# Kernel tuning notes

Hardware: AMD Instinct MI355X
Metric: run time of the kernel (lower is better)

Reference implementation:

```python
import jax, jax.numpy as jnp
import numpy as np

DIM = 512
NUM_HEADS = 8
HEAD_DIM = DIM // NUM_HEADS
SCALE = HEAD_DIM ** -0.5


def setup_inputs() -> dict:
    key = jax.random.key(0)
    k1, k2, k3, k4 = jax.random.split(key, 4)
    x = jax.random.normal(k1, (2, 4096, DIM), dtype=jnp.float32)
    # Linear weights stored as (in, out) for x @ W; torch Linear(dim, 3*dim, bias=False)
    w_qkv = jax.random.normal(k2, (DIM, 3 * DIM), dtype=jnp.float32) * (DIM ** -0.5)
    w_proj = jax.random.normal(k3, (DIM, DIM), dtype=jnp.float32) * (DIM ** -0.5)
    b_proj = jax.random.normal(k4, (DIM,), dtype=jnp.float32) * 0.02
    return {"x": x, "w_qkv": w_qkv, "w_proj": w_proj, "b_proj": b_proj}


def reference(x, w_qkv, w_proj, b_proj):
    B, N, C = x.shape
    qkv = (x @ w_qkv).reshape(B, N, 3, NUM_HEADS, HEAD_DIM)
    qkv = jnp.transpose(qkv, (2, 0, 3, 1, 4))  # (3, B, H, N, hd)
    q, k, v = qkv[0], qkv[1], qkv[2]
    attn = jnp.einsum("bhnd,bhmd->bhnm", q, k) * SCALE
    attn = jax.nn.softmax(attn, axis=-1)
    out = jnp.einsum("bhnm,bhmd->bhnd", attn, v)
    out = jnp.transpose(out, (0, 2, 1, 3)).reshape(B, N, C)
    return out @ w_proj + b_proj
```

## Files before the change

### kernel.cpp

```cpp
#include <hip/hip_runtime.h>
#include <hip/hip_bf16.h>
#include <stdint.h>
#include <math.h>

#define NC3 1536
#define QSCALE 0.18033688011111907f
#define KSPLIT 2

typedef __attribute__((ext_vector_type(8))) short short8;
typedef __attribute__((ext_vector_type(4))) short short4v;
typedef __attribute__((ext_vector_type(4))) float f32x4;
typedef __attribute__((ext_vector_type(16))) float f32x16;
typedef __attribute__((ext_vector_type(8))) _Float16 f16x8;
typedef __attribute__((ext_vector_type(2))) __fp16 fp16x2;

static __device__ __forceinline__ short f2bf(float f) {
    union { __hip_bfloat16 h; short s; } u;
    u.h = __float2bfloat16(f);
    return u.s;
}
static __device__ __forceinline__ float bf2f(short s) {
    return __uint_as_float(((unsigned)(unsigned short)s) << 16);
}
static __device__ __forceinline__ unsigned bfpack(float a, float b) {
    unsigned ua = (__float_as_uint(a) + 0x8000u) >> 16;
    unsigned ub = (__float_as_uint(b) + 0x8000u) & 0xffff0000u;
    return ua | ub;
}
static __device__ __forceinline__ unsigned hpack(float a, float b) {
    union { fp16x2 h; unsigned u; } c;
    c.h = __builtin_amdgcn_cvt_pkrtz(a, b);
    return c.u;
}

#define GLD_LDS(g, l)                                                          \
    __builtin_amdgcn_global_load_lds(                                          \
        (const __attribute__((address_space(1))) void*)(g),                    \
        (__attribute__((address_space(3))) void*)(l), 16, 0, 0)

__global__ __launch_bounds__(256) void cast_f32_bf16(const float* __restrict__ src,
                                                     short* __restrict__ dst, int n4) {
    int i = blockIdx.x * 256 + threadIdx.x;
    if (i < n4) {
        float4 v = ((const float4*)src)[i];
        short4v o = {f2bf(v.x), f2bf(v.y), f2bf(v.z), f2bf(v.w)};
        ((short4v*)dst)[i] = o;
    }
}

__global__ __launch_bounds__(256) void transpose_weights(const float* __restrict__ wqkv,
                                                         short* __restrict__ wqkvT,
                                                         const float* __restrict__ wproj,
                                                         short* __restrict__ wprojT) {
    const float* src;
    short* dst;
    int C;
    if (blockIdx.z == 0) { src = wqkv; dst = wqkvT; C = 1536; }
    else                 { if (blockIdx.x >= 16) return; src = wproj; dst = wprojT; C = 512; }
    const int R = 512;
    __shared__ short t[32][33];
    int c0 = blockIdx.x * 32, r0 = blockIdx.y * 32;
    int tx = threadIdx.x, ty = threadIdx.y;
#pragma unroll
    for (int i = 0; i < 4; i++)
        t[ty + i * 8][tx] = f2bf(src[(size_t)(r0 + ty + i * 8) * C + c0 + tx]);
    __syncthreads();
#pragma unroll
    for (int i = 0; i < 4; i++)
        dst[(size_t)(c0 + ty + i * 8) * R + r0 + tx] = t[tx][ty + i * 8];
}

__global__ __launch_bounds__(256) void transpose_v(const short* __restrict__ QKV,
                                                   short* __restrict__ VT) {
    __shared__ short t[32][33];
    int n0 = blockIdx.x * 32, d0 = blockIdx.y * 32;
    int bh = blockIdx.z;
    int b = bh >> 3, h = bh & 7;
    const short* src = QKV + (size_t)b * 4096 * NC3 + 1024 + h * 64;
    short* dst = VT + (size_t)bh * 64 * 4096;
    int tx = threadIdx.x, ty = threadIdx.y;
#pragma unroll
    for (int i = 0; i < 4; i++)
        t[ty + i * 8][tx] = src[(size_t)(n0 + ty + i * 8) * NC3 + d0 + tx];
    __syncthreads();
    int ptx = (tx & ~12) | ((tx & 4) << 1) | ((tx & 8) >> 1);
#pragma unroll
    for (int i = 0; i < 4; i++) {
        union { __fp16 h; short s; } cv;
        cv.h = (__fp16)bf2f(t[tx][ty + i * 8]);
        dst[(size_t)(d0 + ty + i * 8) * 4096 + n0 + ptx] = cv.s;
    }
}

__global__ __launch_bounds__(256) void combine_partials(const short* __restrict__ Op0,
                                                        const short* __restrict__ Op1,
                                                        const float* __restrict__ lp,
                                                        short* __restrict__ AO) {
    int i = (blockIdx.x * 256 + threadIdx.x) * 8;
    int row = i >> 9;
    int h = (i >> 6) & 7;
    float linv = 1.0f / (lp[row * 8 + h] + lp[65536 + row * 8 + h]);
    short8 a = *(const short8*)(Op0 + i);
    short8 b = *(const short8*)(Op1 + i);
    short8 o;
#pragma unroll
    for (int j = 0; j < 8; j++)
        o[j] = f2bf((bf2f(a[j]) + bf2f(b[j])) * linv);
    *(short8*)(AO + i) = o;
}

template <int NMODE, int NTILE>
__global__ __launch_bounds__(256) void gemm128(const short* __restrict__ A,
                                               const short* __restrict__ Bt,
                                               short* __restrict__ OutB,
                                               float* __restrict__ OutF,
                                               const float* __restrict__ bias) {
    constexpr int NI = NTILE / 32;
    __shared__ __attribute__((aligned(16))) short a_sm[128 * 64];
    __shared__ __attribute__((aligned(16))) short b_sm[NTILE * 64];
    const int tid = threadIdx.x;
    const int lane = tid & 63;
    const int wave = tid >> 6;
    const int wr = wave >> 1, wc = wave & 1;
    const int quad = lane >> 4;
    const int l15 = lane & 15;
    const int m0 = blockIdx.x * 128;
    const int n0 = blockIdx.y * NTILE;
    const int srow = lane >> 3;
    const int schunk = (lane & 7) ^ srow;

    f32x4 zero4 = {0.f, 0.f, 0.f, 0.f};
    f32x4 acc[4][NI];
#pragma unroll
    for (int i = 0; i < 4; i++)
#pragma unroll
        for (int j = 0; j < NI; j++) acc[i][j] = zero4;

    for (int k0 = 0; k0 < 512; k0 += 64) {
        __syncthreads();
#pragma unroll
        for (int i = 0; i < 4; i++) {
            int r0 = wave * 32 + i * 8;
            const short* ga = A + (size_t)(m0 + r0 + srow) * 512 + k0 + schunk * 8;
            GLD_LDS(ga, a_sm + r0 * 64);
        }
#pragma unroll
        for (int i = 0; i < NTILE / 32; i++) {
            int r0 = wave * (NTILE / 4) + i * 8;
            const short* gb = Bt + (size_t)(n0 + r0 + srow) * 512 + k0 + schunk * 8;
            GLD_LDS(gb, b_sm + r0 * 64);
        }
        __syncthreads();
#pragma unroll
        for (int kk = 0; kk < 2; kk++) {
            short8 af[4], bfr[NI];
#pragma unroll
            for (int mi = 0; mi < 4; mi++) {
                int row = wr * 64 + mi * 16 + l15;
                int slot = (kk * 4 + quad) ^ (row & 7);
                af[mi] = *(const short8*)(a_sm + row * 64 + slot * 8);
            }
#pragma unroll
            for (int ni = 0; ni < NI; ni++) {
                int row = wc * (NTILE / 2) + ni * 16 + l15;
                int slot = (kk * 4 + quad) ^ (row & 7);
                bfr[ni] = *(const short8*)(b_sm + row * 64 + slot * 8);
            }
#pragma unroll
            for (int mi = 0; mi < 4; mi++)
#pragma unroll
                for (int ni = 0; ni < NI; ni++)
                    acc[mi][ni] = __builtin_amdgcn_mfma_f32_16x16x32_bf16(
                        af[mi], bfr[ni], acc[mi][ni], 0, 0, 0);
        }
    }

#pragma unroll
    for (int mi = 0; mi < 4; mi++) {
#pragma unroll
        for (int ni = 0; ni < NI; ni++) {
            int gm0 = m0 + wr * 64 + mi * 16 + quad * 4;
            int gn = n0 + wc * (NTILE / 2) + ni * 16 + l15;
            f32x4 v = acc[mi][ni];
#pragma unroll
            for (int r = 0; r < 4; r++) {
                int gm = gm0 + r;
                float val = v[r];
                if (NMODE == 0) {
                    float o = (gn < 512) ? val * QSCALE : val;
                    OutB[(size_t)gm * NC3 + gn] = f2bf(o);
                } else {
                    OutF[(size_t)gm * 512 + gn] = val + bias[gn];
                }
            }
        }
    }
}

__global__ __launch_bounds__(256, 4) void attn_kernel(const short* __restrict__ QKV,
                                                      const short* __restrict__ VT,
                                                      short* __restrict__ Op0,
                                                      short* __restrict__ Op1,
                                                      float* __restrict__ lpart) {
    __shared__ __attribute__((aligned(16))) short k_sm[2][64 * 64];
    __shared__ __attribute__((aligned(16))) short v_sm[2][64 * 64];

    const int tid = threadIdx.x;
    const int lane = tid & 63;
    const int wave = tid >> 6;
    const int l31 = lane & 31;
    const int hi = lane >> 5;
    const int qt = blockIdx.x;
    const int bh = blockIdx.y;
    const int ks = blockIdx.z;
    const int b = bh >> 3, h = bh & 7;
    const size_t tokbase = (size_t)b * 4096;
    const int rowbase = qt * 128;
    const int kt0 = ks * (64 / KSPLIT);
    const int kt1 = kt0 + (64 / KSPLIT);
    const short* Qg = QKV + h * 64;
    const short* Kg = QKV + 512 + h * 64;
    const short* VTg = VT + (size_t)bh * 64 * 4096;
    const int srow = lane >> 3;
    const int schunk = (lane & 7) ^ srow;

    short* qstage = &k_sm[0][0];
#pragma unroll
    for (int i = 0; i < 4; i++) {
        int r0 = wave * 32 + i * 8;
        GLD_LDS(Qg + (tokbase + rowbase + r0 + srow) * NC3 + schunk * 8, qstage + r0 * 64);
    }
    __syncthreads();
    const int qrow = wave * 32 + l31;
    short8 qf[4];
#pragma unroll
    for (int kk = 0; kk < 4; kk++) {
        int slot = (kk * 2 + hi) ^ (qrow & 7);
        qf[kk] = *(const short8*)(qstage + qrow * 64 + slot * 8);
    }
    __syncthreads();

#pragma unroll
    for (int i = 0; i < 2; i++) {
        int r0 = wave * 16 + i * 8;
        GLD_LDS(Kg + (tokbase + (size_t)kt0 * 64 + r0 + srow) * NC3 + schunk * 8,
                k_sm[0] + r0 * 64);
        GLD_LDS(VTg + (size_t)(r0 + srow) * 4096 + kt0 * 64 + schunk * 8,
                v_sm[0] + r0 * 64);
    }

    const _Float16 onef = (_Float16)1.0f;
    const f16x8 ones16 = {onef, onef, onef, onef, onef, onef, onef, onef};

    f32x16 acc_o[2], acc_l;
#pragma unroll
    for (int i = 0; i < 16; i++) { acc_o[0][i] = 0.f; acc_o[1][i] = 0.f; acc_l[i] = 0.f; }

    for (int kt = kt0; kt < kt1; kt++) {
        __syncthreads();
        const int cur = kt & 1;
        if (kt < kt1 - 1) {
            const int nb = cur ^ 1;
#pragma unroll
            for (int i = 0; i < 2; i++) {
                int r0 = wave * 16 + i * 8;
                GLD_LDS(Kg + (tokbase + (size_t)(kt + 1) * 64 + r0 + srow) * NC3 + schunk * 8,
                        k_sm[nb] + r0 * 64);
                GLD_LDS(VTg + (size_t)(r0 + srow) * 4096 + (kt + 1) * 64 + schunk * 8,
                        v_sm[nb] + r0 * 64);
            }
        }

        f32x16 s[2];
#pragma unroll
        for (int i = 0; i < 16; i++) { s[0][i] = 0.f; s[1][i] = 0.f; }
#pragma unroll
        for (int kk = 0; kk < 4; kk++) {
#pragma unroll
            for (int kb = 0; kb < 2; kb++) {
                int row = kb * 32 + l31;
                int slot = (kk * 2 + hi) ^ (row & 7);
                short8 kf = *(const short8*)(k_sm[cur] + row * 64 + slot * 8);
                s[kb] = __builtin_amdgcn_mfma_f32_32x32x16_bf16(kf, qf[kk], s[kb], 0, 0, 0);
            }
        }

        unsigned pk[2][8];
#pragma unroll
        for (int kb = 0; kb < 2; kb++)
#pragma unroll
            for (int i = 0; i < 16; i += 2)
                pk[kb][i >> 1] = hpack(__builtin_amdgcn_exp2f(s[kb][i]),
                                       __builtin_amdgcn_exp2f(s[kb][i + 1]));

#pragma unroll
        for (int g = 0; g < 4; g++) {
            union { unsigned u[4]; f16x8 v; } pf;
#pragma unroll
            for (int t = 0; t < 4; t++) pf.u[t] = pk[g >> 1][4 * (g & 1) + t];
            acc_l = __builtin_amdgcn_mfma_f32_32x32x16_f16(ones16, pf.v, acc_l, 0, 0, 0);
#pragma unroll
            for (int db = 0; db < 2; db++) {
                int row = db * 32 + l31;
                int slot = (g * 2 + hi) ^ (row & 7);
                f16x8 vf = *(const f16x8*)(v_sm[cur] + row * 64 + slot * 8);
                acc_o[db] = __builtin_amdgcn_mfma_f32_32x32x16_f16(vf, pf.v, acc_o[db], 0, 0, 0);
            }
        }
    }

    __syncthreads();

    size_t growq = tokbase + rowbase + qrow;
    if (hi == 0) lpart[(size_t)ks * 65536 + growq * 8 + h] = acc_l[0];

    short* osm = &k_sm[0][0] + wave * 2048;
#pragma unroll
    for (int db = 0; db < 2; db++) {
#pragma unroll
        for (int i = 0; i < 16; i += 2) {
            int d = db * 32 + (i & 3) + 8 * (i >> 2) + 4 * hi;
            unsigned pkd = bfpack(acc_o[db][i], acc_o[db][i + 1]);
            int slot = (d >> 3) ^ (l31 & 7);
            *(unsigned*)(osm + l31 * 64 + slot * 8 + (d & 7)) = pkd;
        }
    }
    short* Od = (ks == 0) ? Op0 : Op1;
#pragma unroll
    for (int j = 0; j < 4; j++) {
        int r = lane >> 1;
        int c = (lane & 1) * 4 + j;
        int slot = c ^ (r & 7);
        short8 ov = *(const short8*)(osm + r * 64 + slot * 8);
        size_t grow = tokbase + rowbase + wave * 32 + r;
        *(short8*)(Od + grow * 512 + h * 64 + c * 8) = ov;
    }
}

extern "C" void kernel_launch(void* const* d_in, const int* in_sizes, int n_in,
                              void* d_out, int out_size, void* d_ws, size_t ws_size,
                              hipStream_t stream) {
    (void)in_sizes; (void)n_in; (void)out_size; (void)ws_size;
    const float* x = (const float*)d_in[0];
    const float* wqkv = (const float*)d_in[1];
    const float* wproj = (const float*)d_in[2];
    const float* bproj = (const float*)d_in[3];
    float* out = (float*)d_out;

    short* ws = (short*)d_ws;
    short* xbf = ws;
    short* wqkvT = xbf + (size_t)4194304;
    short* wprojT = wqkvT + (size_t)1536 * 512;
    short* QKV = wprojT + (size_t)512 * 512;
    short* VTb = QKV + (size_t)8192 * 1536;
    short* AO = VTb + (size_t)16 * 64 * 4096;
    short* Opart1 = xbf;
    float* lpart = (float*)wqkvT;

    cast_f32_bf16<<<4096, 256, 0, stream>>>(x, xbf, 1048576);
    transpose_weights<<<dim3(48, 16, 2), dim3(32, 8), 0, stream>>>(wqkv, wqkvT, wproj, wprojT);
    gemm128<0, 128><<<dim3(64, 12), 256, 0, stream>>>(xbf, wqkvT, QKV, nullptr, nullptr);
    transpose_v<<<dim3(128, 2, 16), dim3(32, 8), 0, stream>>>(QKV, VTb);
    attn_kernel<<<dim3(32, 16, KSPLIT), 256, 0, stream>>>(QKV, VTb, AO, Opart1, lpart);
    combine_partials<<<2048, 256, 0, stream>>>(AO, Opart1, lpart, AO);
    gemm128<1, 64><<<dim3(64, 8), 256, 0, stream>>>(AO, wprojT, nullptr, out, bproj);
}
```

Measured before the change: 203.2 us.

## Fuse split-K combine into projection GEMM and merge prep kernels

```diff
diff --git a/kernel.cpp b/kernel.cpp
--- a/kernel.cpp
+++ b/kernel.cpp
@@ -22,10 +22,10 @@
 static __device__ __forceinline__ float bf2f(short s) {
     return __uint_as_float(((unsigned)(unsigned short)s) << 16);
 }
-static __device__ __forceinline__ unsigned bfpack(float a, float b) {
-    unsigned ua = (__float_as_uint(a) + 0x8000u) >> 16;
-    unsigned ub = (__float_as_uint(b) + 0x8000u) & 0xffff0000u;
-    return ua | ub;
+static __device__ __forceinline__ short f2h(float f) {
+    union { __fp16 h; short s; } u;
+    u.h = (__fp16)f;
+    return u.s;
 }
 static __device__ __forceinline__ unsigned hpack(float a, float b) {
     union { fp16x2 h; unsigned u; } c;
@@ -38,36 +38,43 @@
         (const __attribute__((address_space(1))) void*)(g),                    \
         (__attribute__((address_space(3))) void*)(l), 16, 0, 0)
 
-__global__ __launch_bounds__(256) void cast_f32_bf16(const float* __restrict__ src,
-                                                     short* __restrict__ dst, int n4) {
-    int i = blockIdx.x * 256 + threadIdx.x;
-    if (i < n4) {
-        float4 v = ((const float4*)src)[i];
-        short4v o = {f2bf(v.x), f2bf(v.y), f2bf(v.z), f2bf(v.w)};
-        ((short4v*)dst)[i] = o;
-    }
-}
-
-__global__ __launch_bounds__(256) void transpose_weights(const float* __restrict__ wqkv,
-                                                         short* __restrict__ wqkvT,
-                                                         const float* __restrict__ wproj,
-                                                         short* __restrict__ wprojT) {
+#define GSTRIDE 520
+#define LADDR(row, slot) ((((row) >> 3) * GSTRIDE) + (((row) & 7) * 64) + (slot) * 8)
+
+__global__ __launch_bounds__(256) void prep(const float* __restrict__ x,
+                                            short* __restrict__ xbf,
+                                            const float* __restrict__ wqkv,
+                                            short* __restrict__ wqkvT,
+                                            const float* __restrict__ wproj,
+                                            short* __restrict__ wprojT) {
+    int tx = threadIdx.x, ty = threadIdx.y;
+    int tid = ty * 32 + tx;
+    if (blockIdx.z == 0) {
+        int bid = blockIdx.y * 48 + blockIdx.x;
+        for (int i = bid * 256 + tid; i < 1048576; i += 768 * 256) {
+            float4 v = ((const float4*)x)[i];
+            short4v o = {f2bf(v.x), f2bf(v.y), f2bf(v.z), f2bf(v.w)};
+            ((short4v*)xbf)[i] = o;
+        }
+        return;
+    }
     const float* src;
     short* dst;
     int C;
-    if (blockIdx.z == 0) { src = wqkv; dst = wqkvT; C = 1536; }
-    else                 { if (blockIdx.x >= 16) return; src = wproj; dst = wprojT; C = 512; }
-    const int R = 512;
+    bool tof16;
+    if (blockIdx.z == 1) { src = wqkv; dst = wqkvT; C = 1536; tof16 = false; }
+    else                 { if (blockIdx.x >= 16) return; src = wproj; dst = wprojT; C = 512; tof16 = true; }
     __shared__ short t[32][33];
     int c0 = blockIdx.x * 32, r0 = blockIdx.y * 32;
-    int tx = threadIdx.x, ty = threadIdx.y;
+#pragma unroll
+    for (int i = 0; i < 4; i++) {
+        float v = src[(size_t)(r0 + ty + i * 8) * C + c0 + tx];
+        t[ty + i * 8][tx] = tof16 ? f2h(v) : f2bf(v);
+    }
+    __syncthreads();
 #pragma unroll
     for (int i = 0; i < 4; i++)
-        t[ty + i * 8][tx] = f2bf(src[(size_t)(r0 + ty + i * 8) * C + c0 + tx]);
-    __syncthreads();
-#pragma unroll
-    for (int i = 0; i < 4; i++)
-        dst[(size_t)(c0 + ty + i * 8) * R + r0 + tx] = t[tx][ty + i * 8];
+        dst[(size_t)(c0 + ty + i * 8) * 512 + r0 + tx] = t[tx][ty + i * 8];
 }
 
 __global__ __launch_bounds__(256) void transpose_v(const short* __restrict__ QKV,
@@ -85,39 +92,15 @@
     __syncthreads();
     int ptx = (tx & ~12) | ((tx & 4) << 1) | ((tx & 8) >> 1);
 #pragma unroll
-    for (int i = 0; i < 4; i++) {
-        union { __fp16 h; short s; } cv;
-        cv.h = (__fp16)bf2f(t[tx][ty + i * 8]);
-        dst[(size_t)(d0 + ty + i * 8) * 4096 + n0 + ptx] = cv.s;
-    }
-}
-
-__global__ __launch_bounds__(256) void combine_partials(const short* __restrict__ Op0,
-                                                        const short* __restrict__ Op1,
-                                                        const float* __restrict__ lp,
-                                                        short* __restrict__ AO) {
-    int i = (blockIdx.x * 256 + threadIdx.x) * 8;
-    int row = i >> 9;
-    int h = (i >> 6) & 7;
-    float linv = 1.0f / (lp[row * 8 + h] + lp[65536 + row * 8 + h]);
-    short8 a = *(const short8*)(Op0 + i);
-    short8 b = *(const short8*)(Op1 + i);
-    short8 o;
-#pragma unroll
-    for (int j = 0; j < 8; j++)
-        o[j] = f2bf((bf2f(a[j]) + bf2f(b[j])) * linv);
-    *(short8*)(AO + i) = o;
-}
-
-template <int NMODE, int NTILE>
-__global__ __launch_bounds__(256) void gemm128(const short* __restrict__ A,
-                                               const short* __restrict__ Bt,
-                                               short* __restrict__ OutB,
-                                               float* __restrict__ OutF,
-                                               const float* __restrict__ bias) {
-    constexpr int NI = NTILE / 32;
+    for (int i = 0; i < 4; i++)
+        dst[(size_t)(d0 + ty + i * 8) * 4096 + n0 + ptx] = f2h(bf2f(t[tx][ty + i * 8]));
+}
+
+__global__ __launch_bounds__(256) void gemm_qkv(const short* __restrict__ A,
+                                                const short* __restrict__ Bt,
+                                                short* __restrict__ Out) {
     __shared__ __attribute__((aligned(16))) short a_sm[128 * 64];
-    __shared__ __attribute__((aligned(16))) short b_sm[NTILE * 64];
+    __shared__ __attribute__((aligned(16))) short b_sm[128 * 64];
     const int tid = threadIdx.x;
     const int lane = tid & 63;
     const int wave = tid >> 6;
@@ -125,51 +108,43 @@
     const int quad = lane >> 4;
     const int l15 = lane & 15;
     const int m0 = blockIdx.x * 128;
-    const int n0 = blockIdx.y * NTILE;
+    const int n0 = blockIdx.y * 128;
     const int srow = lane >> 3;
     const int schunk = (lane & 7) ^ srow;
 
     f32x4 zero4 = {0.f, 0.f, 0.f, 0.f};
-    f32x4 acc[4][NI];
+    f32x4 acc[4][4];
 #pragma unroll
     for (int i = 0; i < 4; i++)
 #pragma unroll
-        for (int j = 0; j < NI; j++) acc[i][j] = zero4;
+        for (int j = 0; j < 4; j++) acc[i][j] = zero4;
 
     for (int k0 = 0; k0 < 512; k0 += 64) {
         __syncthreads();
 #pragma unroll
         for (int i = 0; i < 4; i++) {
             int r0 = wave * 32 + i * 8;
-            const short* ga = A + (size_t)(m0 + r0 + srow) * 512 + k0 + schunk * 8;
-            GLD_LDS(ga, a_sm + r0 * 64);
-        }
-#pragma unroll
-        for (int i = 0; i < NTILE / 32; i++) {
-            int r0 = wave * (NTILE / 4) + i * 8;
-            const short* gb = Bt + (size_t)(n0 + r0 + srow) * 512 + k0 + schunk * 8;
-            GLD_LDS(gb, b_sm + r0 * 64);
+            GLD_LDS(A + (size_t)(m0 + r0 + srow) * 512 + k0 + schunk * 8, a_sm + r0 * 64);
+            GLD_LDS(Bt + (size_t)(n0 + r0 + srow) * 512 + k0 + schunk * 8, b_sm + r0 * 64);
         }
         __syncthreads();
 #pragma unroll
         for (int kk = 0; kk < 2; kk++) {
-            short8 af[4], bfr[NI];
+            short8 af[4], bfr[4];
 #pragma unroll
             for (int mi = 0; mi < 4; mi++) {
                 int row = wr * 64 + mi * 16 + l15;
-                int slot = (kk * 4 + quad) ^ (row & 7);
-                af[mi] = *(const short8*)(a_sm + row * 64 + slot * 8);
-            }
-#pragma unroll
-            for (int ni = 0; ni < NI; ni++) {
-                int row = wc * (NTILE / 2) + ni * 16 + l15;
-                int slot = (kk * 4 + quad) ^ (row & 7);
-                bfr[ni] = *(const short8*)(b_sm + row * 64 + slot * 8);
+                af[mi] = *(const short8*)(a_sm + row * 64 + (((kk * 4 + quad) ^ (row & 7))) * 8);
+            }
+#pragma unroll
+            for (int ni = 0; ni < 4; ni++) {
+                int row = wc * 64 + ni * 16 + l15;
+                bfr[ni] = *(const short8*)(b_sm + row * 64 + (((kk * 4 + quad) ^ (row & 7))) * 8);
             }
 #pragma unroll
             for (int mi = 0; mi < 4; mi++)
 #pragma unroll
-                for (int ni = 0; ni < NI; ni++)
+                for (int ni = 0; ni < 4; ni++)
                     acc[mi][ni] = __builtin_amdgcn_mfma_f32_16x16x32_bf16(
                         af[mi], bfr[ni], acc[mi][ni], 0, 0, 0);
         }
@@ -178,20 +153,15 @@
 #pragma unroll
     for (int mi = 0; mi < 4; mi++) {
 #pragma unroll
-        for (int ni = 0; ni < NI; ni++) {
+        for (int ni = 0; ni < 4; ni++) {
             int gm0 = m0 + wr * 64 + mi * 16 + quad * 4;
-            int gn = n0 + wc * (NTILE / 2) + ni * 16 + l15;
+            int gn = n0 + wc * 64 + ni * 16 + l15;
             f32x4 v = acc[mi][ni];
 #pragma unroll
             for (int r = 0; r < 4; r++) {
-                int gm = gm0 + r;
                 float val = v[r];
-                if (NMODE == 0) {
-                    float o = (gn < 512) ? val * QSCALE : val;
-                    OutB[(size_t)gm * NC3 + gn] = f2bf(o);
-                } else {
-                    OutF[(size_t)gm * 512 + gn] = val + bias[gn];
-                }
+                float o = (gn < 512) ? val * QSCALE : val;
+                Out[(size_t)(gm0 + r) * NC3 + gn] = f2bf(o);
             }
         }
     }
@@ -202,8 +172,8 @@
                                                       short* __restrict__ Op0,
                                                       short* __restrict__ Op1,
                                                       float* __restrict__ lpart) {
-    __shared__ __attribute__((aligned(16))) short k_sm[2][64 * 64];
-    __shared__ __attribute__((aligned(16))) short v_sm[2][64 * 64];
+    __shared__ __attribute__((aligned(16))) short k_sm[2][8 * GSTRIDE];
+    __shared__ __attribute__((aligned(16))) short v_sm[2][8 * GSTRIDE];
 
     const int tid = threadIdx.x;
     const int lane = tid & 63;
@@ -228,7 +198,8 @@
 #pragma unroll
     for (int i = 0; i < 4; i++) {
         int r0 = wave * 32 + i * 8;
-        GLD_LDS(Qg + (tokbase + rowbase + r0 + srow) * NC3 + schunk * 8, qstage + r0 * 64);
+        GLD_LDS(Qg + (tokbase + rowbase + r0 + srow) * NC3 + schunk * 8,
+                qstage + (r0 >> 3) * GSTRIDE);
     }
     __syncthreads();
     const int qrow = wave * 32 + l31;
@@ -236,7 +207,7 @@
 #pragma unroll
     for (int kk = 0; kk < 4; kk++) {
         int slot = (kk * 2 + hi) ^ (qrow & 7);
-        qf[kk] = *(const short8*)(qstage + qrow * 64 + slot * 8);
+        qf[kk] = *(const short8*)(qstage + LADDR(qrow, slot));
     }
     __syncthreads();
 
@@ -244,9 +215,9 @@
     for (int i = 0; i < 2; i++) {
         int r0 = wave * 16 + i * 8;
         GLD_LDS(Kg + (tokbase + (size_t)kt0 * 64 + r0 + srow) * NC3 + schunk * 8,
-                k_sm[0] + r0 * 64);
+                k_sm[0] + (r0 >> 3) * GSTRIDE);
         GLD_LDS(VTg + (size_t)(r0 + srow) * 4096 + kt0 * 64 + schunk * 8,
-                v_sm[0] + r0 * 64);
+                v_sm[0] + (r0 >> 3) * GSTRIDE);
     }
 
     const _Float16 onef = (_Float16)1.0f;
@@ -265,9 +236,9 @@
             for (int i = 0; i < 2; i++) {
                 int r0 = wave * 16 + i * 8;
                 GLD_LDS(Kg + (tokbase + (size_t)(kt + 1) * 64 + r0 + srow) * NC3 + schunk * 8,
-                        k_sm[nb] + r0 * 64);
+                        k_sm[nb] + (r0 >> 3) * GSTRIDE);
                 GLD_LDS(VTg + (size_t)(r0 + srow) * 4096 + (kt + 1) * 64 + schunk * 8,
-                        v_sm[nb] + r0 * 64);
+                        v_sm[nb] + (r0 >> 3) * GSTRIDE);
             }
         }
 
@@ -280,7 +251,7 @@
             for (int kb = 0; kb < 2; kb++) {
                 int row = kb * 32 + l31;
                 int slot = (kk * 2 + hi) ^ (row & 7);
-                short8 kf = *(const short8*)(k_sm[cur] + row * 64 + slot * 8);
+                short8 kf = *(const short8*)(k_sm[cur] + LADDR(row, slot));
                 s[kb] = __builtin_amdgcn_mfma_f32_32x32x16_bf16(kf, qf[kk], s[kb], 0, 0, 0);
             }
         }
@@ -303,7 +274,7 @@
             for (int db = 0; db < 2; db++) {
                 int row = db * 32 + l31;
                 int slot = (g * 2 + hi) ^ (row & 7);
-                f16x8 vf = *(const f16x8*)(v_sm[cur] + row * 64 + slot * 8);
+                f16x8 vf = *(const f16x8*)(v_sm[cur] + LADDR(row, slot));
                 acc_o[db] = __builtin_amdgcn_mfma_f32_32x32x16_f16(vf, pf.v, acc_o[db], 0, 0, 0);
             }
         }
@@ -320,7 +291,7 @@
 #pragma unroll
         for (int i = 0; i < 16; i += 2) {
             int d = db * 32 + (i & 3) + 8 * (i >> 2) + 4 * hi;
-            unsigned pkd = bfpack(acc_o[db][i], acc_o[db][i + 1]);
+            unsigned pkd = hpack(acc_o[db][i], acc_o[db][i + 1]);
             int slot = (d >> 3) ^ (l31 & 7);
             *(unsigned*)(osm + l31 * 64 + slot * 8 + (d & 7)) = pkd;
         }
@@ -334,6 +305,101 @@
         short8 ov = *(const short8*)(osm + r * 64 + slot * 8);
         size_t grow = tokbase + rowbase + wave * 32 + r;
         *(short8*)(Od + grow * 512 + h * 64 + c * 8) = ov;
+    }
+}
+
+__global__ __launch_bounds__(256) void gemm_proj(const short* __restrict__ Op0,
+                                                 const short* __restrict__ Op1,
+                                                 const float* __restrict__ lpart,
+                                                 const short* __restrict__ Bt,
+                                                 float* __restrict__ OutF,
+                                                 const float* __restrict__ bias) {
+    __shared__ __attribute__((aligned(16))) short a0_sm[128 * 64];
+    __shared__ __attribute__((aligned(16))) short a1_sm[128 * 64];
+    __shared__ __attribute__((aligned(16))) short b_sm[64 * 64];
+    __shared__ float linv_sm[128 * 8];
+    const int tid = threadIdx.x;
+    const int lane = tid & 63;
+    const int wave = tid >> 6;
+    const int wr = wave >> 1, wc = wave & 1;
+    const int quad = lane >> 4;
+    const int l15 = lane & 15;
+    const int m0 = blockIdx.x * 128;
+    const int n0 = blockIdx.y * 64;
+    const int srow = lane >> 3;
+    const int schunk = (lane & 7) ^ srow;
+
+    {
+        int idx = tid * 4;
+        int row = idx >> 3;
+        int hh = idx & 7;
+        float4 va = *(const float4*)(lpart + (size_t)(m0 + row) * 8 + hh);
+        float4 vb = *(const float4*)(lpart + 65536 + (size_t)(m0 + row) * 8 + hh);
+        linv_sm[idx + 0] = 1.0f / (va.x + vb.x);
+        linv_sm[idx + 1] = 1.0f / (va.y + vb.y);
+        linv_sm[idx + 2] = 1.0f / (va.z + vb.z);
+        linv_sm[idx + 3] = 1.0f / (va.w + vb.w);
+    }
+
+    f32x4 zero4 = {0.f, 0.f, 0.f, 0.f};
+    f32x4 acc[4][2];
+#pragma unroll
+    for (int i = 0; i < 4; i++) { acc[i][0] = zero4; acc[i][1] = zero4; }
+
+    for (int k0 = 0; k0 < 512; k0 += 64) {
+        __syncthreads();
+#pragma unroll
+        for (int i = 0; i < 4; i++) {
+            int r0 = wave * 32 + i * 8;
+            GLD_LDS(Op0 + (size_t)(m0 + r0 + srow) * 512 + k0 + schunk * 8, a0_sm + r0 * 64);
+            GLD_LDS(Op1 + (size_t)(m0 + r0 + srow) * 512 + k0 + schunk * 8, a1_sm + r0 * 64);
+        }
+#pragma unroll
+        for (int i = 0; i < 2; i++) {
+            int r0 = wave * 16 + i * 8;
+            GLD_LDS(Bt + (size_t)(n0 + r0 + srow) * 512 + k0 + schunk * 8, b_sm + r0 * 64);
+        }
+        __syncthreads();
+        const int h = k0 >> 6;
+#pragma unroll
+        for (int kk = 0; kk < 2; kk++) {
+            f16x8 af[4], bfr[2];
+#pragma unroll
+            for (int mi = 0; mi < 4; mi++) {
+                int row = wr * 64 + mi * 16 + l15;
+                int slot = (kk * 4 + quad) ^ (row & 7);
+                f16x8 a0v = *(const f16x8*)(a0_sm + row * 64 + slot * 8);
+                f16x8 a1v = *(const f16x8*)(a1_sm + row * 64 + slot * 8);
+                _Float16 lh = (_Float16)linv_sm[row * 8 + h];
+                f16x8 lv = {lh, lh, lh, lh, lh, lh, lh, lh};
+                af[mi] = (a0v + a1v) * lv;
+            }
+#pragma unroll
+            for (int ni = 0; ni < 2; ni++) {
+                int row = wc * 32 + ni * 16 + l15;
+                int slot = (kk * 4 + quad) ^ (row & 7);
+                bfr[ni] = *(const f16x8*)(b_sm + row * 64 + slot * 8);
+            }
+#pragma unroll
+            for (int mi = 0; mi < 4; mi++)
+#pragma unroll
+                for (int ni = 0; ni < 2; ni++)
+                    acc[mi][ni] = __builtin_amdgcn_mfma_f32_16x16x32_f16(
+                        af[mi], bfr[ni], acc[mi][ni], 0, 0, 0);
+        }
+    }
+
+#pragma unroll
+    for (int mi = 0; mi < 4; mi++) {
+#pragma unroll
+        for (int ni = 0; ni < 2; ni++) {
+            int gm0 = m0 + wr * 64 + mi * 16 + quad * 4;
+            int gn = n0 + wc * 32 + ni * 16 + l15;
+            f32x4 v = acc[mi][ni];
+#pragma unroll
+            for (int r = 0; r < 4; r++)
+                OutF[(size_t)(gm0 + r) * 512 + gn] = v[r] + bias[gn];
+        }
     }
 }
 
@@ -353,15 +419,13 @@
     short* wprojT = wqkvT + (size_t)1536 * 512;
     short* QKV = wprojT + (size_t)512 * 512;
     short* VTb = QKV + (size_t)8192 * 1536;
-    short* AO = VTb + (size_t)16 * 64 * 4096;
-    short* Opart1 = xbf;
+    short* Op0 = VTb + (size_t)16 * 64 * 4096;
+    short* Op1 = xbf;
     float* lpart = (float*)wqkvT;
 
-    cast_f32_bf16<<<4096, 256, 0, stream>>>(x, xbf, 1048576);
-    transpose_weights<<<dim3(48, 16, 2), dim3(32, 8), 0, stream>>>(wqkv, wqkvT, wproj, wprojT);
-    gemm128<0, 128><<<dim3(64, 12), 256, 0, stream>>>(xbf, wqkvT, QKV, nullptr, nullptr);
+    prep<<<dim3(48, 16, 3), dim3(32, 8), 0, stream>>>(x, xbf, wqkv, wqkvT, wproj, wprojT);
+    gemm_qkv<<<dim3(64, 12), 256, 0, stream>>>(xbf, wqkvT, QKV);
     transpose_v<<<dim3(128, 2, 16), dim3(32, 8), 0, stream>>>(QKV, VTb);
-    attn_kernel<<<dim3(32, 16, KSPLIT), 256, 0, stream>>>(QKV, VTb, AO, Opart1, lpart);
-    combine_partials<<<2048, 256, 0, stream>>>(AO, Opart1, lpart, AO);
-    gemm128<1, 64><<<dim3(64, 8), 256, 0, stream>>>(AO, wprojT, nullptr, out, bproj);
-}
+    attn_kernel<<<dim3(32, 16, KSPLIT), 256, 0, stream>>>(QKV, VTb, Op0, Op1, lpart);
+    gemm_proj<<<dim3(64, 8), 256, 0, stream>>>(Op0, Op1, lpart, wprojT, out, bproj);
+}
```

Result: no change. 201.4 us (-0.9%).
